# Kernel tuning notes

Hardware: AMD Instinct MI355X
Metric: run time of the kernel (lower is better)

Reference implementation:

```python
import jax, jax.numpy as jnp
import numpy as np

N = 50000      # nodes
E = 800000     # edges (avg degree 16)
F_IN = 256
F_OUT = 256


def setup_inputs() -> dict:
    key = jax.random.key(0)
    ks = jax.random.split(key, 8)
    feature = jax.random.normal(ks[0], (N, F_IN), dtype=jnp.float32)
    e_w = jax.random.uniform(ks[1], (E, 1), dtype=jnp.float32)
    snorm_n = jnp.ones((N, 1), dtype=jnp.float32)
    snorm_e = jnp.ones((E, 1), dtype=jnp.float32)
    src = jax.random.randint(ks[2], (E,), 0, N, dtype=jnp.int32)
    dst = jax.random.randint(ks[3], (E,), 0, N, dtype=jnp.int32)
    scale = 1.0 / np.sqrt(F_IN)
    W_self = jax.random.normal(ks[4], (F_IN, F_OUT), dtype=jnp.float32) * scale
    W = jax.random.normal(ks[5], (F_IN, F_OUT), dtype=jnp.float32) * scale
    b = jax.random.normal(ks[6], (F_OUT,), dtype=jnp.float32) * scale
    return {"feature": feature, "e_w": e_w, "snorm_n": snorm_n,
            "snorm_e": snorm_e, "W_self": W_self, "W": W, "b": b,
            "src": src, "dst": dst}


def reference(feature, e_w, snorm_n, snorm_e, W_self, W, b, src, dst):
    n = feature.shape[0]
    ones_e = jnp.ones_like(src, dtype=feature.dtype)
    # self transform
    h_s = feature @ W_self                                   # [N, F_OUT]
    # source-side degree normalization: deg_out^{-1/2}
    out_deg = jnp.maximum(jax.ops.segment_sum(ones_e, src, num_segments=n), 1.0)
    feat = feature * (out_deg ** -0.5)[:, None]              # [N, F_IN]
    # message = h[src] * e_w, aggregated by sum into dst (u_mul_e + sum reduce)
    msgs = feat[src] * e_w                                   # [E, F_IN]
    agg = jax.ops.segment_sum(msgs, dst, num_segments=n)     # [N, F_IN]
    # neighbor transform + destination-side degree normalization
    h = agg @ W + b                                          # [N, F_OUT]
    in_deg = jnp.maximum(jax.ops.segment_sum(ones_e, dst, num_segments=n), 1.0)
    h = h * (in_deg ** -0.5)[:, None]
    return h_s + h, e_w
```

## Files before the change

### kernel.cpp

```cpp
#include <hip/hip_runtime.h>
#include <hip/hip_bf16.h>

#define N_NODES 50000
#define N_EDGES 800000

#define ROW_TILES    391
#define HIST_BLOCKS  782
#define GEMM_SPACE   1568
#define K1_BLOCKS    (HIST_BLOCKS + GEMM_SPACE)
#define WCONV_BLOCKS 512
#define SCAN_BLOCKS  196
#define EDGE_BLOCKS  782

typedef __bf16 bf16x8_t __attribute__((ext_vector_type(8)));
typedef float  f32x4_t  __attribute__((ext_vector_type(4)));
typedef unsigned short u16x8 __attribute__((ext_vector_type(8)));

__device__ __forceinline__ unsigned short f2bf(float x) {
  __hip_bfloat16 h = __float2bfloat16(x);
  return __builtin_bit_cast(unsigned short, h);
}
__device__ __forceinline__ float bf2f(unsigned short u) {
  unsigned int v = ((unsigned int)u) << 16;
  return __builtin_bit_cast(float, v);
}
__device__ __forceinline__ unsigned int pk2(float lo, float hi) {
  return ((unsigned int)f2bf(hi) << 16) | (unsigned int)f2bf(lo);
}

__global__ __launch_bounds__(256) void wconv_kernel(
    const float* __restrict__ Wself, const float* __restrict__ W,
    unsigned short* __restrict__ Bt)
{
  int idx = blockIdx.x * 256 + threadIdx.x;
  int n = idx >> 8, k = idx & 255;
  float v = (n < 256) ? Wself[k * 256 + n] : W[k * 256 + (n - 256)];
  Bt[idx] = f2bf(v);
}

__global__ __launch_bounds__(256, 4) void gemm_edge_kernel(
    const float* __restrict__ feature,
    const unsigned short* __restrict__ Bt,
    const float* __restrict__ e_w, const int* __restrict__ src, const int* __restrict__ dst,
    int* __restrict__ cnt_in, int* __restrict__ cnt_out,
    unsigned char* __restrict__ rank8, float* __restrict__ out1,
    unsigned short* __restrict__ hs16,
    unsigned char* __restrict__ y8)
{
  const int b   = blockIdx.x;
  const int tid = threadIdx.x;

  if (b < HIST_BLOCKS) {
    const int e0 = b * 1024 + tid;
#pragma unroll
    for (int k = 0; k < 4; ++k) {
      int e = e0 + k * 256;
      if (e < N_EDGES) {
        int s = src[e], d = dst[e];
        out1[e] = e_w[e];
        atomicAdd(&cnt_out[s], 1);
        rank8[e] = (unsigned char)atomicAdd(&cnt_in[d], 1);
      }
    }
    return;
  }

  const int u  = b - HIST_BLOCKS;
  const int q  = (u >> 3) & 3;
  const int t  = (u >> 5) * 8 + (((u & 7) + 6) & 7);
  if (t >= ROW_TILES) return;

  __shared__ __align__(16) unsigned short As[2][128 * 32];
  __shared__ __align__(16) unsigned short Bs[2][128 * 32];

  const int m0   = t * 128;
  const int bn0  = q * 128;
  const int lane = tid & 63;
  const int wave = tid >> 6;
  const int wm   = (wave & 1) * 64;
  const int wn   = (wave >> 1) * 64;
  const int fr   = lane & 15;
  const int fkc  = lane >> 4;

  const int ra = tid >> 1, ha = tid & 1;
  const int sA = (ra >> 1) & 3;
  const int arow = (m0 + ra < N_NODES) ? (m0 + ra) : 0;
  const float* aptr = feature + (size_t)arow * 256 + ha * 16;
  const int aw0 = ra * 32 + (((2 * ha) ^ sA) * 8);
  const int aw1 = ra * 32 + ((((2 * ha) | 1) ^ sA) * 8);

  f32x4_t acc[4][4] = {};

  {
#pragma unroll
    for (int i = 0; i < 2; ++i) {
      int r  = i * 64 + (tid >> 2);
      int cg = (tid & 3) ^ ((r >> 1) & 3);
      const unsigned short* gb = Bt + (size_t)(bn0 + r) * 256 + cg * 8;
      __builtin_amdgcn_global_load_lds((const __attribute__((address_space(1))) void*)gb,
                                       (__attribute__((address_space(3))) void*)&Bs[0][i * 2048 + wave * 512],
                                       16, 0, 0);
    }
    float4 a0 = *(const float4*)(aptr + 0);
    float4 a1 = *(const float4*)(aptr + 4);
    float4 a2 = *(const float4*)(aptr + 8);
    float4 a3 = *(const float4*)(aptr + 12);
    uint4 p0, p1;
    p0.x = pk2(a0.x, a0.y); p0.y = pk2(a0.z, a0.w);
    p0.z = pk2(a1.x, a1.y); p0.w = pk2(a1.z, a1.w);
    p1.x = pk2(a2.x, a2.y); p1.y = pk2(a2.z, a2.w);
    p1.z = pk2(a3.x, a3.y); p1.w = pk2(a3.z, a3.w);
    *(uint4*)&As[0][aw0] = p0;
    *(uint4*)&As[0][aw1] = p1;
  }
  __syncthreads();

#pragma unroll
  for (int s = 0; s < 8; ++s) {
    const int cb = s & 1, nb = cb ^ 1;
    float4 a0, a1, a2, a3;
    if (s < 7) {
      const int k0 = (s + 1) * 32;
#pragma unroll
      for (int i = 0; i < 2; ++i) {
        int r  = i * 64 + (tid >> 2);
        int cg = (tid & 3) ^ ((r >> 1) & 3);
        const unsigned short* gb = Bt + (size_t)(bn0 + r) * 256 + k0 + cg * 8;
        __builtin_amdgcn_global_load_lds((const __attribute__((address_space(1))) void*)gb,
                                         (__attribute__((address_space(3))) void*)&Bs[nb][i * 2048 + wave * 512],
                                         16, 0, 0);
      }
      a0 = *(const float4*)(aptr + k0 + 0);
      a1 = *(const float4*)(aptr + k0 + 4);
      a2 = *(const float4*)(aptr + k0 + 8);
      a3 = *(const float4*)(aptr + k0 + 12);
    }

    bf16x8_t af[4], bv[4];
#pragma unroll
    for (int i = 0; i < 4; ++i) {
      int R = wm + i * 16 + fr;
      af[i] = *(const bf16x8_t*)&As[cb][R * 32 + ((fkc ^ ((R >> 1) & 3)) * 8)];
    }
#pragma unroll
    for (int j = 0; j < 4; ++j) {
      int R = wn + j * 16 + fr;
      bv[j] = *(const bf16x8_t*)&Bs[cb][R * 32 + ((fkc ^ ((R >> 1) & 3)) * 8)];
    }
#pragma unroll
    for (int i = 0; i < 4; ++i)
#pragma unroll
      for (int j = 0; j < 4; ++j)
        acc[i][j] = __builtin_amdgcn_mfma_f32_16x16x32_bf16(af[i], bv[j], acc[i][j], 0, 0, 0);

    if (s < 7) {
      uint4 p0, p1;
      p0.x = pk2(a0.x, a0.y); p0.y = pk2(a0.z, a0.w);
      p0.z = pk2(a1.x, a1.y); p0.w = pk2(a1.z, a1.w);
      p1.x = pk2(a2.x, a2.y); p1.y = pk2(a2.z, a2.w);
      p1.z = pk2(a3.x, a3.y); p1.w = pk2(a3.z, a3.w);
      *(uint4*)&As[nb][aw0] = p0;
      *(uint4*)&As[nb][aw1] = p1;
      __syncthreads();
    }
  }

  if (q < 2) {
    const int cbase = q * 128 + wn + (lane & 15);
#pragma unroll
    for (int i = 0; i < 4; ++i) {
      int rowb = m0 + wm + i * 16 + (lane >> 4) * 4;
#pragma unroll
      for (int j = 0; j < 4; ++j) {
        int col = cbase + j * 16;
#pragma unroll
        for (int r = 0; r < 4; ++r) {
          int row = rowb + r;
          if (row < N_NODES)
            hs16[(size_t)row * 256 + col] = f2bf(acc[i][j][r]);
        }
      }
    }
  } else {
    const int cbase = (q - 2) * 128 + wn + (lane & 15);
#pragma unroll
    for (int i = 0; i < 4; ++i) {
      int rowb = m0 + wm + i * 16 + (lane >> 4) * 4;
#pragma unroll
      for (int j = 0; j < 4; ++j) {
        int col = cbase + j * 16;
#pragma unroll
        for (int r = 0; r < 4; ++r) {
          int row = rowb + r;
          if (row < N_NODES) {
            float ys = acc[i][j][r];
            unsigned int pk = (unsigned int)__builtin_amdgcn_cvt_pk_fp8_f32(ys, ys, 0, false);
            y8[(size_t)row * 256 + col] = (unsigned char)(pk & 0xffu);
          }
        }
      }
    }
  }
}

__global__ __launch_bounds__(256) void scan1_kernel(
    const int* __restrict__ cnt, int* __restrict__ sums)
{
  int idx = blockIdx.x * 256 + threadIdx.x;
  int v = (idx < N_NODES) ? cnt[idx] : 0;
#pragma unroll
  for (int d = 32; d; d >>= 1) v += __shfl_down(v, d);
  __shared__ int sm[4];
  if ((threadIdx.x & 63) == 0) sm[threadIdx.x >> 6] = v;
  __syncthreads();
  if (threadIdx.x == 0) sums[blockIdx.x] = sm[0] + sm[1] + sm[2] + sm[3];
}

__global__ __launch_bounds__(256) void scan2_kernel(int* __restrict__ sums)
{
  const int t = threadIdx.x;
  int v = (t < SCAN_BLOCKS) ? sums[t] : 0;
  __shared__ int sm[256];
  sm[t] = v;
  __syncthreads();
  for (int d = 1; d < 256; d <<= 1) {
    int u = (t >= d) ? sm[t - d] : 0;
    __syncthreads();
    sm[t] += u;
    __syncthreads();
  }
  if (t < SCAN_BLOCKS) sums[t] = sm[t] - v;
}

__global__ __launch_bounds__(256) void scan3_kernel(
    const int* __restrict__ cnt, const int* __restrict__ sums, int* __restrict__ off)
{
  const int t = threadIdx.x;
  int idx = blockIdx.x * 256 + t;
  int v = (idx < N_NODES) ? cnt[idx] : 0;
  __shared__ int sm[256];
  sm[t] = v;
  __syncthreads();
  for (int d = 1; d < 256; d <<= 1) {
    int u = (t >= d) ? sm[t - d] : 0;
    __syncthreads();
    sm[t] += u;
    __syncthreads();
  }
  if (idx <= N_NODES) off[idx] = sm[t] - v + sums[blockIdx.x];
}

__global__ __launch_bounds__(256) void scatter_kernel(
    const float* __restrict__ e_w, const int* __restrict__ src, const int* __restrict__ dst,
    const unsigned char* __restrict__ rank8, const int* __restrict__ off,
    unsigned int* __restrict__ csr)
{
  const int e0 = blockIdx.x * 1024 + threadIdx.x;
#pragma unroll
  for (int k = 0; k < 4; ++k) {
    int e = e0 + k * 256;
    if (e < N_EDGES) {
      int d = dst[e];
      int r = rank8[e];
      float w = e_w[e];
      int s = src[e];
      csr[off[d] + r] = ((unsigned int)f2bf(w) << 16) | (unsigned int)s;
    }
  }
}

__global__ __launch_bounds__(256) void agg_kernel(
    const unsigned char* __restrict__ y8, const unsigned int* __restrict__ csr,
    const int* __restrict__ off, const int* __restrict__ cnt_out,
    const unsigned short* __restrict__ hs16,
    const float* __restrict__ bias, float* __restrict__ out0)
{
  const int hw   = threadIdx.x >> 5;
  const int lane = threadIdx.x & 31;
  const int node = blockIdx.x * 8 + hw;
  if (node >= N_NODES) return;
  const int base = off[node];
  const int deg  = off[node + 1] - base;

  float a0 = 0.f, a1 = 0.f, a2 = 0.f, a3 = 0.f;
  float a4 = 0.f, a5 = 0.f, a6 = 0.f, a7 = 0.f;

  for (int bb = 0; bb < deg; bb += 32) {
    int idx = bb + lane;
    unsigned int ent = (idx < deg) ? csr[base + idx] : 0u;
    int   sl = (int)(ent & 0xffffu);
    float wl = bf2f((unsigned short)(ent >> 16));
    int co = cnt_out[sl]; if (co < 1) co = 1;
    wl *= rsqrtf((float)co);

#pragma unroll
    for (int t0 = 0; t0 < 32; t0 += 16) {
      if (bb + t0 >= deg) break;
#pragma unroll
      for (int t = 0; t < 16; ++t) {
        int eb = t0 + t;
        int   s = __shfl(sl, eb, 32);
        float w = __shfl(wl, eb, 32);
        uint2 u = *(const uint2*)(y8 + (size_t)s * 256 + lane * 8);
        a0 += w * __builtin_amdgcn_cvt_f32_fp8(u.x, 0);
        a1 += w * __builtin_amdgcn_cvt_f32_fp8(u.x, 1);
        a2 += w * __builtin_amdgcn_cvt_f32_fp8(u.x, 2);
        a3 += w * __builtin_amdgcn_cvt_f32_fp8(u.x, 3);
        a4 += w * __builtin_amdgcn_cvt_f32_fp8(u.y, 0);
        a5 += w * __builtin_amdgcn_cvt_f32_fp8(u.y, 1);
        a6 += w * __builtin_amdgcn_cvt_f32_fp8(u.y, 2);
        a7 += w * __builtin_amdgcn_cvt_f32_fp8(u.y, 3);
      }
    }
  }

  int dn = deg < 1 ? 1 : deg;
  float inv = rsqrtf((float)dn);
  size_t offo = (size_t)node * 256 + lane * 8;
  u16x8 hv = *(const u16x8*)(hs16 + offo);
  float4 b0 = *(const float4*)(bias + lane * 8);
  float4 b1 = *(const float4*)(bias + lane * 8 + 4);
  float4 o0, o1;
  o0.x = bf2f(hv[0]) + (a0 + b0.x) * inv;
  o0.y = bf2f(hv[1]) + (a1 + b0.y) * inv;
  o0.z = bf2f(hv[2]) + (a2 + b0.z) * inv;
  o0.w = bf2f(hv[3]) + (a3 + b0.w) * inv;
  o1.x = bf2f(hv[4]) + (a4 + b1.x) * inv;
  o1.y = bf2f(hv[5]) + (a5 + b1.y) * inv;
  o1.z = bf2f(hv[6]) + (a6 + b1.z) * inv;
  o1.w = bf2f(hv[7]) + (a7 + b1.w) * inv;
  *(float4*)(out0 + offo)     = o0;
  *(float4*)(out0 + offo + 4) = o1;
}

extern "C" void kernel_launch(void* const* d_in, const int* in_sizes, int n_in,
                              void* d_out, int out_size, void* d_ws, size_t ws_size,
                              hipStream_t stream) {
  const float* feature = (const float*)d_in[0];
  const float* e_w     = (const float*)d_in[1];
  const float* W_self  = (const float*)d_in[4];
  const float* W       = (const float*)d_in[5];
  const float* bias    = (const float*)d_in[6];
  const int*   src     = (const int*)d_in[7];
  const int*   dst     = (const int*)d_in[8];

  float* out0 = (float*)d_out;
  float* out1 = out0 + (size_t)N_NODES * 256;

  char* ws = (char*)d_ws;
  int*            cnt_in  = (int*)(ws + 0);
  int*            cnt_out = (int*)(ws + 262144);
  int*            off     = (int*)(ws + 524288);
  unsigned char*  rank8   = (unsigned char*)(ws + 786432);
  int*            sums    = (int*)(ws + 1638400);
  unsigned int*   csr     = (unsigned int*)(ws + 1835008);
  unsigned short* Bt      = (unsigned short*)(ws + 5242880);
  unsigned char*  y8      = (unsigned char*)(ws + 5767168);
  unsigned short* hs16    = (unsigned short*)(ws + 18567168);

  hipMemsetAsync(ws, 0, 524288, stream);

  wconv_kernel<<<WCONV_BLOCKS, 256, 0, stream>>>(W_self, W, Bt);
  gemm_edge_kernel<<<K1_BLOCKS, 256, 0, stream>>>(
      feature, Bt, e_w, src, dst, cnt_in, cnt_out, rank8, out1, hs16, y8);
  scan1_kernel<<<SCAN_BLOCKS, 256, 0, stream>>>(cnt_in, sums);
  scan2_kernel<<<1, 256, 0, stream>>>(sums);
  scan3_kernel<<<SCAN_BLOCKS, 256, 0, stream>>>(cnt_in, sums, off);
  scatter_kernel<<<EDGE_BLOCKS, 256, 0, stream>>>(e_w, src, dst, rank8, off, csr);
  agg_kernel<<<(N_NODES + 7) / 8, 256, 0, stream>>>(y8, csr, off, cnt_out, hs16, bias, out0);
}
```

Baseline: 283.5 us.

## Interleave histogram and GEMM blocks, fuse scan kernels, hoist source norm, widen agg lanes

Several changes at once. The fused kernel now interleaves histogram blocks among the GEMM tiles, so atomic-heavy edge work runs alongside the matrix work instead of all being dispatched first. The three-stage scan drops its middle kernel: each scan3 block reduces the earlier block sums itself, at the cost of some redundant reads. The source-degree normalisation moves from the gather loop into the scatter kernel, removing one random cnt_out load per edge from aggregation. The aggregation kernel uses 16 lanes per node with 16-byte fp8 loads, raising work per lane and register use.

```diff
diff --git a/kernel.cpp b/kernel.cpp
--- a/kernel.cpp
+++ b/kernel.cpp
@@ -5,9 +5,7 @@
 #define N_EDGES 800000
 
 #define ROW_TILES    391
-#define HIST_BLOCKS  782
-#define GEMM_SPACE   1568
-#define K1_BLOCKS    (HIST_BLOCKS + GEMM_SPACE)
+#define K1_BLOCKS    2352
 #define WCONV_BLOCKS 512
 #define SCAN_BLOCKS  196
 #define EDGE_BLOCKS  782
@@ -49,9 +47,13 @@
 {
   const int b   = blockIdx.x;
   const int tid = threadIdx.x;
-
-  if (b < HIST_BLOCKS) {
-    const int e0 = b * 1024 + tid;
+  const int p   = b % 48;
+  const int w   = b / 48;
+
+  if (p % 3 == 2) {
+    const int h = w * 16 + p / 3;
+    if (h >= EDGE_BLOCKS) return;
+    const int e0 = h * 1024 + tid;
 #pragma unroll
     for (int k = 0; k < 4; ++k) {
       int e = e0 + k * 256;
@@ -65,13 +67,16 @@
     return;
   }
 
-  const int u  = b - HIST_BLOCKS;
-  const int q  = (u >> 3) & 3;
-  const int t  = (u >> 5) * 8 + (((u & 7) + 6) & 7);
-  if (t >= ROW_TILES) return;
-
   __shared__ __align__(16) unsigned short As[2][128 * 32];
   __shared__ __align__(16) unsigned short Bs[2][128 * 32];
+
+  const int c = p >> 3, r = p & 7;
+  int q = 0;
+#pragma unroll
+  for (int cc = 0; cc < 6; ++cc)
+    if (cc < c && (((8 * cc + r) % 3) != 2)) ++q;
+  const int t = w * 8 + r;
+  if (t >= ROW_TILES) return;
 
   const int m0   = t * 128;
   const int bn0  = q * 128;
@@ -94,9 +99,9 @@
   {
 #pragma unroll
     for (int i = 0; i < 2; ++i) {
-      int r  = i * 64 + (tid >> 2);
-      int cg = (tid & 3) ^ ((r >> 1) & 3);
-      const unsigned short* gb = Bt + (size_t)(bn0 + r) * 256 + cg * 8;
+      int rr = i * 64 + (tid >> 2);
+      int cg = (tid & 3) ^ ((rr >> 1) & 3);
+      const unsigned short* gb = Bt + (size_t)(bn0 + rr) * 256 + cg * 8;
       __builtin_amdgcn_global_load_lds((const __attribute__((address_space(1))) void*)gb,
                                        (__attribute__((address_space(3))) void*)&Bs[0][i * 2048 + wave * 512],
                                        16, 0, 0);
@@ -123,9 +128,9 @@
       const int k0 = (s + 1) * 32;
 #pragma unroll
       for (int i = 0; i < 2; ++i) {
-        int r  = i * 64 + (tid >> 2);
-        int cg = (tid & 3) ^ ((r >> 1) & 3);
-        const unsigned short* gb = Bt + (size_t)(bn0 + r) * 256 + k0 + cg * 8;
+        int rr = i * 64 + (tid >> 2);
+        int cg = (tid & 3) ^ ((rr >> 1) & 3);
+        const unsigned short* gb = Bt + (size_t)(bn0 + rr) * 256 + k0 + cg * 8;
         __builtin_amdgcn_global_load_lds((const __attribute__((address_space(1))) void*)gb,
                                          (__attribute__((address_space(3))) void*)&Bs[nb][i * 2048 + wave * 512],
                                          16, 0, 0);
@@ -174,10 +179,10 @@
       for (int j = 0; j < 4; ++j) {
         int col = cbase + j * 16;
 #pragma unroll
-        for (int r = 0; r < 4; ++r) {
-          int row = rowb + r;
+        for (int rr = 0; rr < 4; ++rr) {
+          int row = rowb + rr;
           if (row < N_NODES)
-            hs16[(size_t)row * 256 + col] = f2bf(acc[i][j][r]);
+            hs16[(size_t)row * 256 + col] = f2bf(acc[i][j][rr]);
         }
       }
     }
@@ -190,10 +195,10 @@
       for (int j = 0; j < 4; ++j) {
         int col = cbase + j * 16;
 #pragma unroll
-        for (int r = 0; r < 4; ++r) {
-          int row = rowb + r;
+        for (int rr = 0; rr < 4; ++rr) {
+          int row = rowb + rr;
           if (row < N_NODES) {
-            float ys = acc[i][j][r];
+            float ys = acc[i][j][rr];
             unsigned int pk = (unsigned int)__builtin_amdgcn_cvt_pk_fp8_f32(ys, ys, 0, false);
             y8[(size_t)row * 256 + col] = (unsigned char)(pk & 0xffu);
           }
@@ -216,12 +221,26 @@
   if (threadIdx.x == 0) sums[blockIdx.x] = sm[0] + sm[1] + sm[2] + sm[3];
 }
 
-__global__ __launch_bounds__(256) void scan2_kernel(int* __restrict__ sums)
+__global__ __launch_bounds__(256) void scan3_kernel(
+    const int* __restrict__ cnt, const int* __restrict__ sums, int* __restrict__ off)
 {
   const int t = threadIdx.x;
-  int v = (t < SCAN_BLOCKS) ? sums[t] : 0;
+  const int b = blockIdx.x;
+  int v = (t < b) ? sums[t] : 0;
+#pragma unroll
+  for (int d = 32; d; d >>= 1) v += __shfl_down(v, d);
+  __shared__ int sm4[4];
+  __shared__ int sbase;
+  if ((t & 63) == 0) sm4[t >> 6] = v;
+  __syncthreads();
+  if (t == 0) sbase = sm4[0] + sm4[1] + sm4[2] + sm4[3];
+  __syncthreads();
+  const int base = sbase;
+
+  int idx = b * 256 + t;
+  int c = (idx < N_NODES) ? cnt[idx] : 0;
   __shared__ int sm[256];
-  sm[t] = v;
+  sm[t] = c;
   __syncthreads();
   for (int d = 1; d < 256; d <<= 1) {
     int u = (t >= d) ? sm[t - d] : 0;
@@ -229,31 +248,13 @@
     sm[t] += u;
     __syncthreads();
   }
-  if (t < SCAN_BLOCKS) sums[t] = sm[t] - v;
-}
-
-__global__ __launch_bounds__(256) void scan3_kernel(
-    const int* __restrict__ cnt, const int* __restrict__ sums, int* __restrict__ off)
-{
-  const int t = threadIdx.x;
-  int idx = blockIdx.x * 256 + t;
-  int v = (idx < N_NODES) ? cnt[idx] : 0;
-  __shared__ int sm[256];
-  sm[t] = v;
-  __syncthreads();
-  for (int d = 1; d < 256; d <<= 1) {
-    int u = (t >= d) ? sm[t - d] : 0;
-    __syncthreads();
-    sm[t] += u;
-    __syncthreads();
-  }
-  if (idx <= N_NODES) off[idx] = sm[t] - v + sums[blockIdx.x];
+  if (idx <= N_NODES) off[idx] = sm[t] - c + base;
 }
 
 __global__ __launch_bounds__(256) void scatter_kernel(
     const float* __restrict__ e_w, const int* __restrict__ src, const int* __restrict__ dst,
     const unsigned char* __restrict__ rank8, const int* __restrict__ off,
-    unsigned int* __restrict__ csr)
+    const int* __restrict__ cnt_out, unsigned int* __restrict__ csr)
 {
   const int e0 = blockIdx.x * 1024 + threadIdx.x;
 #pragma unroll
@@ -262,8 +263,9 @@
     if (e < N_EDGES) {
       int d = dst[e];
       int r = rank8[e];
-      float w = e_w[e];
       int s = src[e];
+      int co = cnt_out[s]; if (co < 1) co = 1;
+      float w = e_w[e] * rsqrtf((float)co);
       csr[off[d] + r] = ((unsigned int)f2bf(w) << 16) | (unsigned int)s;
     }
   }
@@ -271,66 +273,85 @@
 
 __global__ __launch_bounds__(256) void agg_kernel(
     const unsigned char* __restrict__ y8, const unsigned int* __restrict__ csr,
-    const int* __restrict__ off, const int* __restrict__ cnt_out,
-    const unsigned short* __restrict__ hs16,
+    const int* __restrict__ off, const unsigned short* __restrict__ hs16,
     const float* __restrict__ bias, float* __restrict__ out0)
 {
-  const int hw   = threadIdx.x >> 5;
-  const int lane = threadIdx.x & 31;
-  const int node = blockIdx.x * 8 + hw;
+  const int qw   = threadIdx.x >> 4;
+  const int lane = threadIdx.x & 15;
+  const int node = blockIdx.x * 16 + qw;
   if (node >= N_NODES) return;
   const int base = off[node];
   const int deg  = off[node + 1] - base;
 
-  float a0 = 0.f, a1 = 0.f, a2 = 0.f, a3 = 0.f;
-  float a4 = 0.f, a5 = 0.f, a6 = 0.f, a7 = 0.f;
-
-  for (int bb = 0; bb < deg; bb += 32) {
+  float a[16];
+#pragma unroll
+  for (int i = 0; i < 16; ++i) a[i] = 0.f;
+
+  for (int bb = 0; bb < deg; bb += 16) {
     int idx = bb + lane;
     unsigned int ent = (idx < deg) ? csr[base + idx] : 0u;
     int   sl = (int)(ent & 0xffffu);
     float wl = bf2f((unsigned short)(ent >> 16));
-    int co = cnt_out[sl]; if (co < 1) co = 1;
-    wl *= rsqrtf((float)co);
-
-#pragma unroll
-    for (int t0 = 0; t0 < 32; t0 += 16) {
+
+#pragma unroll
+    for (int t0 = 0; t0 < 16; t0 += 8) {
       if (bb + t0 >= deg) break;
 #pragma unroll
-      for (int t = 0; t < 16; ++t) {
+      for (int t = 0; t < 8; ++t) {
         int eb = t0 + t;
-        int   s = __shfl(sl, eb, 32);
-        float w = __shfl(wl, eb, 32);
-        uint2 u = *(const uint2*)(y8 + (size_t)s * 256 + lane * 8);
-        a0 += w * __builtin_amdgcn_cvt_f32_fp8(u.x, 0);
-        a1 += w * __builtin_amdgcn_cvt_f32_fp8(u.x, 1);
-        a2 += w * __builtin_amdgcn_cvt_f32_fp8(u.x, 2);
-        a3 += w * __builtin_amdgcn_cvt_f32_fp8(u.x, 3);
-        a4 += w * __builtin_amdgcn_cvt_f32_fp8(u.y, 0);
-        a5 += w * __builtin_amdgcn_cvt_f32_fp8(u.y, 1);
-        a6 += w * __builtin_amdgcn_cvt_f32_fp8(u.y, 2);
-        a7 += w * __builtin_amdgcn_cvt_f32_fp8(u.y, 3);
+        int   s = __shfl(sl, eb, 16);
+        float w = __shfl(wl, eb, 16);
+        uint4 u = *(const uint4*)(y8 + (size_t)s * 256 + lane * 16);
+        a[0]  += w * __builtin_amdgcn_cvt_f32_fp8(u.x, 0);
+        a[1]  += w * __builtin_amdgcn_cvt_f32_fp8(u.x, 1);
+        a[2]  += w * __builtin_amdgcn_cvt_f32_fp8(u.x, 2);
+        a[3]  += w * __builtin_amdgcn_cvt_f32_fp8(u.x, 3);
+        a[4]  += w * __builtin_amdgcn_cvt_f32_fp8(u.y, 0);
+        a[5]  += w * __builtin_amdgcn_cvt_f32_fp8(u.y, 1);
+        a[6]  += w * __builtin_amdgcn_cvt_f32_fp8(u.y, 2);
+        a[7]  += w * __builtin_amdgcn_cvt_f32_fp8(u.y, 3);
+        a[8]  += w * __builtin_amdgcn_cvt_f32_fp8(u.z, 0);
+        a[9]  += w * __builtin_amdgcn_cvt_f32_fp8(u.z, 1);
+        a[10] += w * __builtin_amdgcn_cvt_f32_fp8(u.z, 2);
+        a[11] += w * __builtin_amdgcn_cvt_f32_fp8(u.z, 3);
+        a[12] += w * __builtin_amdgcn_cvt_f32_fp8(u.w, 0);
+        a[13] += w * __builtin_amdgcn_cvt_f32_fp8(u.w, 1);
+        a[14] += w * __builtin_amdgcn_cvt_f32_fp8(u.w, 2);
+        a[15] += w * __builtin_amdgcn_cvt_f32_fp8(u.w, 3);
       }
     }
   }
 
   int dn = deg < 1 ? 1 : deg;
   float inv = rsqrtf((float)dn);
-  size_t offo = (size_t)node * 256 + lane * 8;
-  u16x8 hv = *(const u16x8*)(hs16 + offo);
-  float4 b0 = *(const float4*)(bias + lane * 8);
-  float4 b1 = *(const float4*)(bias + lane * 8 + 4);
-  float4 o0, o1;
-  o0.x = bf2f(hv[0]) + (a0 + b0.x) * inv;
-  o0.y = bf2f(hv[1]) + (a1 + b0.y) * inv;
-  o0.z = bf2f(hv[2]) + (a2 + b0.z) * inv;
-  o0.w = bf2f(hv[3]) + (a3 + b0.w) * inv;
-  o1.x = bf2f(hv[4]) + (a4 + b1.x) * inv;
-  o1.y = bf2f(hv[5]) + (a5 + b1.y) * inv;
-  o1.z = bf2f(hv[6]) + (a6 + b1.z) * inv;
-  o1.w = bf2f(hv[7]) + (a7 + b1.w) * inv;
-  *(float4*)(out0 + offo)     = o0;
-  *(float4*)(out0 + offo + 4) = o1;
+  size_t offo = (size_t)node * 256 + lane * 16;
+  u16x8 h0 = *(const u16x8*)(hs16 + offo);
+  u16x8 h1 = *(const u16x8*)(hs16 + offo + 8);
+  float4 b0 = *(const float4*)(bias + lane * 16);
+  float4 b1 = *(const float4*)(bias + lane * 16 + 4);
+  float4 b2 = *(const float4*)(bias + lane * 16 + 8);
+  float4 b3 = *(const float4*)(bias + lane * 16 + 12);
+  float4 o0, o1, o2, o3;
+  o0.x = bf2f(h0[0]) + (a[0]  + b0.x) * inv;
+  o0.y = bf2f(h0[1]) + (a[1]  + b0.y) * inv;
+  o0.z = bf2f(h0[2]) + (a[2]  + b0.z) * inv;
+  o0.w = bf2f(h0[3]) + (a[3]  + b0.w) * inv;
+  o1.x = bf2f(h0[4]) + (a[4]  + b1.x) * inv;
+  o1.y = bf2f(h0[5]) + (a[5]  + b1.y) * inv;
+  o1.z = bf2f(h0[6]) + (a[6]  + b1.z) * inv;
+  o1.w = bf2f(h0[7]) + (a[7]  + b1.w) * inv;
+  o2.x = bf2f(h1[0]) + (a[8]  + b2.x) * inv;
+  o2.y = bf2f(h1[1]) + (a[9]  + b2.y) * inv;
+  o2.z = bf2f(h1[2]) + (a[10] + b2.z) * inv;
+  o2.w = bf2f(h1[3]) + (a[11] + b2.w) * inv;
+  o3.x = bf2f(h1[4]) + (a[12] + b3.x) * inv;
+  o3.y = bf2f(h1[5]) + (a[13] + b3.y) * inv;
+  o3.z = bf2f(h1[6]) + (a[14] + b3.z) * inv;
+  o3.w = bf2f(h1[7]) + (a[15] + b3.w) * inv;
+  *(float4*)(out0 + offo)      = o0;
+  *(float4*)(out0 + offo + 4)  = o1;
+  *(float4*)(out0 + offo + 8)  = o2;
+  *(float4*)(out0 + offo + 12) = o3;
 }
 
 extern "C" void kernel_launch(void* const* d_in, const int* in_sizes, int n_in,
@@ -364,8 +385,7 @@
   gemm_edge_kernel<<<K1_BLOCKS, 256, 0, stream>>>(
       feature, Bt, e_w, src, dst, cnt_in, cnt_out, rank8, out1, hs16, y8);
   scan1_kernel<<<SCAN_BLOCKS, 256, 0, stream>>>(cnt_in, sums);
-  scan2_kernel<<<1, 256, 0, stream>>>(sums);
   scan3_kernel<<<SCAN_BLOCKS, 256, 0, stream>>>(cnt_in, sums, off);
-  scatter_kernel<<<EDGE_BLOCKS, 256, 0, stream>>>(e_w, src, dst, rank8, off, csr);
-  agg_kernel<<<(N_NODES + 7) / 8, 256, 0, stream>>>(y8, csr, off, cnt_out, hs16, bias, out0);
-}
+  scatter_kernel<<<EDGE_BLOCKS, 256, 0, stream>>>(e_w, src, dst, rank8, off, cnt_out, csr);
+  agg_kernel<<<(N_NODES + 15) / 16, 256, 0, stream>>>(y8, csr, off, hs16, bias, out0);
+}
```

After: 254.5 us. -10.2%, faster.
